# Kernel optimization log

Measured on AMD Instinct MI355X. Metric: run time of the kernel, lower is better.

## Reference

```python
import jax, jax.numpy as jnp
import numpy as np

DIM = 2048
N_HEADS = 16
N_KV_HEADS = 4
HEAD_DIM = DIM // N_HEADS  # 128
N_REP = N_HEADS // N_KV_HEADS  # 4
SEQ = 2048
BATCH = 2


def apply_rope(x, cos, sin):
    # x: [b, s, h, d]; cos/sin: [s, d//2]
    xr = x[..., 0::2]
    xi = x[..., 1::2]
    c = cos[None, :, None, :]
    s = sin[None, :, None, :]
    out_r = xr * c - xi * s
    out_i = xr * s + xi * c
    # interleave back: stack on last axis then flatten
    out = jnp.stack([out_r, out_i], axis=-1)
    return out.reshape(x.shape)


def setup_inputs() -> dict:
    key = jax.random.key(0)
    ks = jax.random.split(key, 7)
    x = jax.random.normal(ks[0], (BATCH, SEQ, DIM), dtype=jnp.float32)
    # realistic rotary tables
    inv_freq = 1.0 / (10000.0 ** (np.arange(0, HEAD_DIM, 2, dtype=np.float32) / HEAD_DIM))
    t = np.arange(SEQ, dtype=np.float32)
    freqs = np.outer(t, inv_freq)  # [S, d//2]
    freqs_cos = jnp.asarray(np.cos(freqs))
    freqs_sin = jnp.asarray(np.sin(freqs))
    sc = 0.02
    Wq = jax.random.normal(ks[1], (DIM, N_HEADS * HEAD_DIM), dtype=jnp.float32) * sc
    Wk = jax.random.normal(ks[2], (DIM, N_KV_HEADS * HEAD_DIM), dtype=jnp.float32) * sc
    Wv = jax.random.normal(ks[3], (DIM, N_KV_HEADS * HEAD_DIM), dtype=jnp.float32) * sc
    Wo = jax.random.normal(ks[4], (N_HEADS * HEAD_DIM, DIM), dtype=jnp.float32) * sc
    return {"x": x, "freqs_cos": freqs_cos, "freqs_sin": freqs_sin,
            "Wq": Wq, "Wk": Wk, "Wv": Wv, "Wo": Wo}


def reference(x, freqs_cos, freqs_sin, Wq, Wk, Wv, Wo):
    b, s, _ = x.shape
    xq = (x @ Wq).reshape(b, s, N_HEADS, HEAD_DIM)
    xk = (x @ Wk).reshape(b, s, N_KV_HEADS, HEAD_DIM)
    xv = (x @ Wv).reshape(b, s, N_KV_HEADS, HEAD_DIM)
    xq = apply_rope(xq, freqs_cos, freqs_sin)
    xk = apply_rope(xk, freqs_cos, freqs_sin)
    # GQA attention without materializing repeated KV:
    # group query heads as [b, g, r, s, d] with g=N_KV_HEADS, r=N_REP
    q = xq.reshape(b, s, N_KV_HEADS, N_REP, HEAD_DIM)
    scale = 1.0 / jnp.sqrt(jnp.float32(HEAD_DIM))
    scores = jnp.einsum('bqgrd,bkgd->bgrqk', q, xk) * scale  # [b,g,r,s,s]
    causal = jnp.tril(jnp.ones((s, s), dtype=bool))
    scores = jnp.where(causal[None, None, None], scores, jnp.finfo(scores.dtype).min)
    probs = jax.nn.softmax(scores, axis=-1)
    out = jnp.einsum('bgrqk,bkgd->bqgrd', probs, xv)  # [b,s,g,r,d]
    out = out.reshape(b, s, N_HEADS * HEAD_DIM)
    return out @ Wo
```

## Files before the change

### kernel.cpp

```cpp
#include <hip/hip_runtime.h>
#include <stdint.h>
#include <stddef.h>

constexpr int BATCH = 2;
constexpr int SEQ   = 2048;
constexpr int EMB   = 2048;
constexpr int HEADS = 16;
constexpr int GQA   = 4;
constexpr int HDIM  = 128;
constexpr int NQKV  = 3072;
constexpr int VOFF  = 2560;
constexpr int MROWS = BATCH * SEQ;

typedef _Float16 half8  __attribute__((ext_vector_type(8)));
typedef _Float16 half4v __attribute__((ext_vector_type(4)));
typedef float    floatx4 __attribute__((ext_vector_type(4)));

__device__ __forceinline__ void st_c(float* p, float v)    { *p = v; }
__device__ __forceinline__ void st_c(_Float16* p, float v) { *p = (_Float16)v; }

__device__ __forceinline__ void gld16(const _Float16* g, _Float16* l) {
    __builtin_amdgcn_global_load_lds(
        (const __attribute__((address_space(1))) void*)g,
        (__attribute__((address_space(3))) void*)l, 16, 0, 0);
}

__global__ void cast_x_kernel(const float* __restrict__ x, _Float16* __restrict__ xh) {
    int i = (blockIdx.x * 256 + threadIdx.x) * 4;
    float4 v = *(const float4*)(x + i);
    half4v h;
    h[0] = (_Float16)v.x; h[1] = (_Float16)v.y; h[2] = (_Float16)v.z; h[3] = (_Float16)v.w;
    *(half4v*)(xh + i) = h;
}

__global__ void transpose_cast(const float* __restrict__ in, _Float16* __restrict__ out,
                               int R, int C) {
    __shared__ float tile[32][33];
    int cb = blockIdx.x * 32, rb = blockIdx.y * 32;
    int tx = threadIdx.x, ty = threadIdx.y;
    #pragma unroll
    for (int j = 0; j < 32; j += 8)
        tile[ty + j][tx] = in[(size_t)(rb + ty + j) * C + (cb + tx)];
    __syncthreads();
    #pragma unroll
    for (int j = 0; j < 32; j += 8)
        out[(size_t)(cb + ty + j) * R + (rb + tx)] = (_Float16)tile[tx][ty + j];
}

template <typename CT, bool ROPE>
__global__ __launch_bounds__(256) void gemm_bt(const _Float16* __restrict__ A,
                                               const _Float16* __restrict__ Bt,
                                               CT* __restrict__ C,
                                               int M, int N, int K,
                                               const float* __restrict__ fc,
                                               const float* __restrict__ fs) {
    constexpr int LDT = 40;
    __shared__ _Float16 As[128 * LDT];
    __shared__ _Float16 Bs[128 * LDT];
    const int tid  = threadIdx.x;
    const int bm   = blockIdx.y * 128, bn = blockIdx.x * 128;
    const int lane = tid & 63, wid = tid >> 6;
    const int wr   = wid >> 1, wc = wid & 1;
    const int qd   = lane >> 4, m15 = lane & 15;

    const int sr = tid >> 2;
    const int sc = (tid & 3) * 8;
    const _Float16* Ag  = A  + (size_t)(bm + sr) * K + sc;
    const _Float16* Ag2 = Ag + (size_t)64 * K;
    const _Float16* Bg  = Bt + (size_t)(bn + sr) * K + sc;
    const _Float16* Bg2 = Bg + (size_t)64 * K;

    half8 a0 = *(const half8*)(Ag);
    half8 a1 = *(const half8*)(Ag2);
    half8 b0 = *(const half8*)(Bg);
    half8 b1 = *(const half8*)(Bg2);

    floatx4 acc[4][4] = {};

    _Float16* AsW  = As + sr * LDT + sc;
    _Float16* AsW2 = AsW + 64 * LDT;
    _Float16* BsW  = Bs + sr * LDT + sc;
    _Float16* BsW2 = BsW + 64 * LDT;
    const _Float16* AsR = As + (wr * 64 + m15) * LDT + qd * 8;
    const _Float16* BsR = Bs + (wc * 64 + m15) * LDT + qd * 8;

    for (int k0 = 0; k0 < K; k0 += 32) {
        *(half8*)AsW  = a0;  *(half8*)AsW2 = a1;
        *(half8*)BsW  = b0;  *(half8*)BsW2 = b1;
        __syncthreads();
        if (k0 + 32 < K) {
            a0 = *(const half8*)(Ag  + k0 + 32);
            a1 = *(const half8*)(Ag2 + k0 + 32);
            b0 = *(const half8*)(Bg  + k0 + 32);
            b1 = *(const half8*)(Bg2 + k0 + 32);
        }
        half8 af[4], bf[4];
        #pragma unroll
        for (int i = 0; i < 4; i++) af[i] = *(const half8*)(AsR + i * 16 * LDT);
        #pragma unroll
        for (int i = 0; i < 4; i++) bf[i] = *(const half8*)(BsR + i * 16 * LDT);
        #pragma unroll
        for (int mi = 0; mi < 4; mi++)
            #pragma unroll
            for (int ni = 0; ni < 4; ni++)
                acc[mi][ni] = __builtin_amdgcn_mfma_f32_16x16x32_f16(af[mi], bf[ni], acc[mi][ni], 0, 0, 0);
        __syncthreads();
    }

    #pragma unroll
    for (int mi = 0; mi < 4; mi++)
        #pragma unroll
        for (int ni = 0; ni < 4; ni++)
            #pragma unroll
            for (int r = 0; r < 4; r++) {
                int row = bm + wr * 64 + mi * 16 + qd * 4 + r;
                int col = bn + wc * 64 + ni * 16 + m15;
                float v = acc[mi][ni][r];
                if (ROPE && col < VOFF) {
                    int si = row & (SEQ - 1);
                    int fi = (col >> 1) & 63;
                    float c  = fc[si * 64 + fi];
                    float sn = fs[si * 64 + fi];
                    float other = __shfl_xor(v, 1, 64);
                    v = (m15 & 1) ? (v * c + other * sn) : (v * c - other * sn);
                }
                st_c(&C[(size_t)row * N + col], v);
            }
}

__global__ void transpose_v(const _Float16* __restrict__ qkv, _Float16* __restrict__ vt) {
    __shared__ _Float16 tile[32][33];
    int sb = blockIdx.x * 32, db = blockIdx.y * 32;
    int bg = blockIdx.z;
    int tx = threadIdx.x, ty = threadIdx.y;
    const _Float16* src = qkv + (size_t)(bg >> 2) * SEQ * NQKV + VOFF + (bg & 3) * HDIM;
    #pragma unroll
    for (int j = 0; j < 32; j += 8)
        tile[ty + j][tx] = src[(size_t)(sb + ty + j) * NQKV + db + tx];
    __syncthreads();
    _Float16* dst = vt + (size_t)bg * HDIM * SEQ;
    #pragma unroll
    for (int j = 0; j < 32; j += 8)
        dst[(size_t)(db + ty + j) * SEQ + sb + tx] = tile[tx][ty + j];
}

__global__ __launch_bounds__(256, 1) void flash_attn(const _Float16* __restrict__ qkv,
                                                     const _Float16* __restrict__ vt,
                                                     _Float16* __restrict__ ob) {
    const int bx   = blockIdx.x;
    const int g    = blockIdx.y;
    const int b    = blockIdx.z;
    const int tid  = threadIdx.x;
    const int lane = tid & 63, wid = tid >> 6;
    const int h    = g * 4 + wid;
    const int qd   = lane >> 4, m15 = lane & 15;

    __shared__ _Float16 Ks[2][64 * 128];
    __shared__ _Float16 Vs[2][128 * 64];
    __shared__ _Float16 Ps[4][32 * 64];

    const _Float16* kg = qkv + (size_t)(b * SEQ) * NQKV + EMB + g * HDIM;
    const _Float16* vg = vt + (size_t)(b * GQA + g) * HDIM * SEQ;
    _Float16* pw = Ps[wid];

    const int kl = lane >> 4, kc16 = lane & 15;
    const int vl = lane >> 3, vc8  = lane & 7;
    const _Float16* kgp[4]; const _Float16* vgp[4];
    int ksoff[4], vsoff[4];
    #pragma unroll
    for (int j = 0; j < 4; j++) {
        int t = wid * 4 + j;
        int kr = t * 4 + kl;
        kgp[j] = kg + (size_t)kr * NQKV + ((kc16 ^ (kr & 15)) * 8);
        ksoff[j] = t * 512;
        int vr = t * 8 + vl;
        vgp[j] = vg + (size_t)vr * SEQ + ((vc8 ^ (vr & 7)) * 8);
        vsoff[j] = t * 512;
    }

    half8 ones;
    #pragma unroll
    for (int i = 0; i < 8; i++) ones[i] = (_Float16)1.0f;
    const _Float16 qsc = (_Float16)(0.08838834764831845f * 1.44269504088896341f);

    for (int ph = 0; ph < 2; ++ph) {
        const int sidx   = ph ? bx : 63 - bx;
        const int q0     = sidx * 32;
        const int ktLast = sidx >> 1;

        __syncthreads();
        #pragma unroll
        for (int j = 0; j < 4; j++) gld16(kgp[j], &Ks[0][ksoff[j]]);
        #pragma unroll
        for (int j = 0; j < 4; j++) gld16(vgp[j], &Vs[0][vsoff[j]]);

        half8 qf[2][4];
        #pragma unroll
        for (int su = 0; su < 2; su++) {
            const _Float16* qb = qkv + (size_t)(b * SEQ + q0 + su * 16 + m15) * NQKV + h * HDIM + qd * 8;
            #pragma unroll
            for (int kc = 0; kc < 4; kc++) {
                half8 q = *(const half8*)(qb + kc * 32);
                #pragma unroll
                for (int i = 0; i < 8; i++) q[i] = (_Float16)(q[i] * qsc);
                qf[su][kc] = q;
            }
        }

        floatx4 o[2][9] = {};

        for (int kt = 0; kt <= ktLast; ++kt) {
            const int cur = kt & 1;
            __syncthreads();
            if (kt < ktLast) {
                const int nb = cur ^ 1;
                const size_t ko = (size_t)(kt + 1) * 64;
                #pragma unroll
                for (int j = 0; j < 4; j++) gld16(kgp[j] + ko * NQKV, &Ks[nb][ksoff[j]]);
                #pragma unroll
                for (int j = 0; j < 4; j++) gld16(vgp[j] + ko, &Vs[nb][vsoff[j]]);
            }
            const _Float16* ksb = Ks[cur];
            const _Float16* vsb = Vs[cur];

            floatx4 sa[2][4] = {};
            #pragma unroll
            for (int nt = 0; nt < 4; ++nt) {
                const int kr = nt * 16 + m15;
                #pragma unroll
                for (int kc = 0; kc < 4; ++kc) {
                    half8 kf = *(const half8*)(&ksb[kr * 128 + (((kc * 4 + qd) ^ (kr & 15)) * 8)]);
                    sa[0][nt] = __builtin_amdgcn_mfma_f32_16x16x32_f16(qf[0][kc], kf, sa[0][nt], 0, 0, 0);
                    sa[1][nt] = __builtin_amdgcn_mfma_f32_16x16x32_f16(qf[1][kc], kf, sa[1][nt], 0, 0, 0);
                }
            }

            const bool diag = (kt == ktLast);
            const int  k0   = kt * 64;
            #pragma unroll
            for (int su = 0; su < 2; su++)
                #pragma unroll
                for (int r = 0; r < 4; r++) {
                    const int prow = su * 16 + qd * 4 + r;
                    #pragma unroll
                    for (int nt = 0; nt < 4; nt++) {
                        float p = __builtin_exp2f(sa[su][nt][r]);
                        if (diag && (k0 + nt * 16 + m15 > q0 + prow)) p = 0.f;
                        int chunk = (nt * 2 + (m15 >> 3)) ^ (prow & 7);
                        pw[prow * 64 + chunk * 8 + (m15 & 7)] = (_Float16)p;
                    }
                }

            half8 pf[2][2];
            #pragma unroll
            for (int su = 0; su < 2; su++)
                #pragma unroll
                for (int kc = 0; kc < 2; kc++) {
                    int prow = su * 16 + m15;
                    pf[su][kc] = *(const half8*)(&pw[prow * 64 + (((kc * 4 + qd) ^ (prow & 7)) * 8)]);
                }
            #pragma unroll
            for (int dt = 0; dt < 8; dt++) {
                const int vr = dt * 16 + m15;
                #pragma unroll
                for (int kc = 0; kc < 2; kc++) {
                    half8 vf = *(const half8*)(&vsb[vr * 64 + (((kc * 4 + qd) ^ (vr & 7)) * 8)]);
                    o[0][dt] = __builtin_amdgcn_mfma_f32_16x16x32_f16(pf[0][kc], vf, o[0][dt], 0, 0, 0);
                    o[1][dt] = __builtin_amdgcn_mfma_f32_16x16x32_f16(pf[1][kc], vf, o[1][dt], 0, 0, 0);
                }
            }
            #pragma unroll
            for (int su = 0; su < 2; su++) {
                o[su][8] = __builtin_amdgcn_mfma_f32_16x16x32_f16(pf[su][0], ones, o[su][8], 0, 0, 0);
                o[su][8] = __builtin_amdgcn_mfma_f32_16x16x32_f16(pf[su][1], ones, o[su][8], 0, 0, 0);
            }
        }

        #pragma unroll
        for (int su = 0; su < 2; su++) {
            float linv[4];
            #pragma unroll
            for (int r = 0; r < 4; r++) linv[r] = 1.0f / o[su][8][r];
            _Float16* od = ob + (size_t)(b * SEQ + q0 + su * 16) * EMB + h * HDIM;
            #pragma unroll
            for (int dt = 0; dt < 8; dt++)
                #pragma unroll
                for (int r = 0; r < 4; r++)
                    od[(size_t)(qd * 4 + r) * EMB + dt * 16 + m15] = (_Float16)(o[su][dt][r] * linv[r]);
        }
    }
}

extern "C" void kernel_launch(void* const* d_in, const int* in_sizes, int n_in,
                              void* d_out, int out_size, void* d_ws, size_t ws_size,
                              hipStream_t stream) {
    (void)in_sizes; (void)n_in; (void)out_size; (void)ws_size;
    const float* x  = (const float*)d_in[0];
    const float* fc = (const float*)d_in[1];
    const float* fs = (const float*)d_in[2];
    const float* Wq = (const float*)d_in[3];
    const float* Wk = (const float*)d_in[4];
    const float* Wv = (const float*)d_in[5];
    const float* Wo = (const float*)d_in[6];
    float* out = (float*)d_out;

    _Float16* Xb   = (_Float16*)d_ws;
    _Float16* Wqkv = Xb   + (size_t)MROWS * EMB;
    _Float16* WoT  = Wqkv + (size_t)NQKV * EMB;
    _Float16* C1   = WoT  + (size_t)EMB * EMB;
    _Float16* Vt   = Wqkv;
    _Float16* Ob   = Xb;

    dim3 tb(32, 8);
    cast_x_kernel<<<MROWS * EMB / 1024, 256, 0, stream>>>(x, Xb);
    transpose_cast<<<dim3(EMB / 32, EMB / 32), tb, 0, stream>>>(Wq, Wqkv, EMB, EMB);
    transpose_cast<<<dim3(512 / 32, EMB / 32), tb, 0, stream>>>(Wk, Wqkv + (size_t)EMB * EMB, EMB, 512);
    transpose_cast<<<dim3(512 / 32, EMB / 32), tb, 0, stream>>>(Wv, Wqkv + (size_t)VOFF * EMB, EMB, 512);
    transpose_cast<<<dim3(EMB / 32, EMB / 32), tb, 0, stream>>>(Wo, WoT, EMB, EMB);

    gemm_bt<_Float16, true><<<dim3(NQKV / 128, MROWS / 128), 256, 0, stream>>>(
        Xb, Wqkv, C1, MROWS, NQKV, EMB, fc, fs);
    transpose_v<<<dim3(SEQ / 32, HDIM / 32, BATCH * GQA), tb, 0, stream>>>(C1, Vt);
    flash_attn<<<dim3(32, GQA, BATCH), 256, 0, stream>>>(C1, Vt, Ob);
    gemm_bt<float, false><<<dim3(EMB / 128, MROWS / 128), 256, 0, stream>>>(
        Ob, WoT, out, MROWS, EMB, EMB, nullptr, nullptr);
}
```

Before: 351.9 us.

## Split flash attention query rows across 8 waves per block

```diff
diff --git a/kernel.cpp b/kernel.cpp
--- a/kernel.cpp
+++ b/kernel.cpp
@@ -144,7 +144,7 @@
         dst[(size_t)(db + ty + j) * SEQ + sb + tx] = tile[tx][ty + j];
 }
 
-__global__ __launch_bounds__(256, 1) void flash_attn(const _Float16* __restrict__ qkv,
+__global__ __launch_bounds__(512, 2) void flash_attn(const _Float16* __restrict__ qkv,
                                                      const _Float16* __restrict__ vt,
                                                      _Float16* __restrict__ ob) {
     const int bx   = blockIdx.x;
@@ -152,12 +152,13 @@
     const int b    = blockIdx.z;
     const int tid  = threadIdx.x;
     const int lane = tid & 63, wid = tid >> 6;
-    const int h    = g * 4 + wid;
+    const int h    = g * 4 + (wid & 3);
+    const int su   = wid >> 2;
     const int qd   = lane >> 4, m15 = lane & 15;
 
     __shared__ _Float16 Ks[2][64 * 128];
     __shared__ _Float16 Vs[2][128 * 64];
-    __shared__ _Float16 Ps[4][32 * 64];
+    __shared__ _Float16 Ps[8][16 * 64];
 
     const _Float16* kg = qkv + (size_t)(b * SEQ) * NQKV + EMB + g * HDIM;
     const _Float16* vg = vt + (size_t)(b * GQA + g) * HDIM * SEQ;
@@ -165,11 +166,11 @@
 
     const int kl = lane >> 4, kc16 = lane & 15;
     const int vl = lane >> 3, vc8  = lane & 7;
-    const _Float16* kgp[4]; const _Float16* vgp[4];
-    int ksoff[4], vsoff[4];
-    #pragma unroll
-    for (int j = 0; j < 4; j++) {
-        int t = wid * 4 + j;
+    const _Float16* kgp[2]; const _Float16* vgp[2];
+    int ksoff[2], vsoff[2];
+    #pragma unroll
+    for (int j = 0; j < 2; j++) {
+        int t = wid * 2 + j;
         int kr = t * 4 + kl;
         kgp[j] = kg + (size_t)kr * NQKV + ((kc16 ^ (kr & 15)) * 8);
         ksoff[j] = t * 512;
@@ -190,24 +191,23 @@
 
         __syncthreads();
         #pragma unroll
-        for (int j = 0; j < 4; j++) gld16(kgp[j], &Ks[0][ksoff[j]]);
-        #pragma unroll
-        for (int j = 0; j < 4; j++) gld16(vgp[j], &Vs[0][vsoff[j]]);
-
-        half8 qf[2][4];
-        #pragma unroll
-        for (int su = 0; su < 2; su++) {
+        for (int j = 0; j < 2; j++) gld16(kgp[j], &Ks[0][ksoff[j]]);
+        #pragma unroll
+        for (int j = 0; j < 2; j++) gld16(vgp[j], &Vs[0][vsoff[j]]);
+
+        half8 qf[4];
+        {
             const _Float16* qb = qkv + (size_t)(b * SEQ + q0 + su * 16 + m15) * NQKV + h * HDIM + qd * 8;
             #pragma unroll
             for (int kc = 0; kc < 4; kc++) {
                 half8 q = *(const half8*)(qb + kc * 32);
                 #pragma unroll
                 for (int i = 0; i < 8; i++) q[i] = (_Float16)(q[i] * qsc);
-                qf[su][kc] = q;
+                qf[kc] = q;
             }
         }
 
-        floatx4 o[2][9] = {};
+        floatx4 o[9] = {};
 
         for (int kt = 0; kt <= ktLast; ++kt) {
             const int cur = kt & 1;
@@ -216,78 +216,66 @@
                 const int nb = cur ^ 1;
                 const size_t ko = (size_t)(kt + 1) * 64;
                 #pragma unroll
-                for (int j = 0; j < 4; j++) gld16(kgp[j] + ko * NQKV, &Ks[nb][ksoff[j]]);
-                #pragma unroll
-                for (int j = 0; j < 4; j++) gld16(vgp[j] + ko, &Vs[nb][vsoff[j]]);
+                for (int j = 0; j < 2; j++) gld16(kgp[j] + ko * NQKV, &Ks[nb][ksoff[j]]);
+                #pragma unroll
+                for (int j = 0; j < 2; j++) gld16(vgp[j] + ko, &Vs[nb][vsoff[j]]);
             }
             const _Float16* ksb = Ks[cur];
             const _Float16* vsb = Vs[cur];
 
-            floatx4 sa[2][4] = {};
+            floatx4 sa[4] = {};
             #pragma unroll
             for (int nt = 0; nt < 4; ++nt) {
                 const int kr = nt * 16 + m15;
                 #pragma unroll
                 for (int kc = 0; kc < 4; ++kc) {
                     half8 kf = *(const half8*)(&ksb[kr * 128 + (((kc * 4 + qd) ^ (kr & 15)) * 8)]);
-                    sa[0][nt] = __builtin_amdgcn_mfma_f32_16x16x32_f16(qf[0][kc], kf, sa[0][nt], 0, 0, 0);
-                    sa[1][nt] = __builtin_amdgcn_mfma_f32_16x16x32_f16(qf[1][kc], kf, sa[1][nt], 0, 0, 0);
+                    sa[nt] = __builtin_amdgcn_mfma_f32_16x16x32_f16(qf[kc], kf, sa[nt], 0, 0, 0);
                 }
             }
 
             const bool diag = (kt == ktLast);
             const int  k0   = kt * 64;
             #pragma unroll
-            for (int su = 0; su < 2; su++)
-                #pragma unroll
-                for (int r = 0; r < 4; r++) {
-                    const int prow = su * 16 + qd * 4 + r;
-                    #pragma unroll
-                    for (int nt = 0; nt < 4; nt++) {
-                        float p = __builtin_exp2f(sa[su][nt][r]);
-                        if (diag && (k0 + nt * 16 + m15 > q0 + prow)) p = 0.f;
-                        int chunk = (nt * 2 + (m15 >> 3)) ^ (prow & 7);
-                        pw[prow * 64 + chunk * 8 + (m15 & 7)] = (_Float16)p;
-                    }
+            for (int r = 0; r < 4; r++) {
+                const int prow = qd * 4 + r;
+                const int rowg = q0 + su * 16 + prow;
+                #pragma unroll
+                for (int nt = 0; nt < 4; nt++) {
+                    float p = __builtin_exp2f(sa[nt][r]);
+                    if (diag && (k0 + nt * 16 + m15 > rowg)) p = 0.f;
+                    int chunk = (nt * 2 + (m15 >> 3)) ^ (prow & 7);
+                    pw[prow * 64 + chunk * 8 + (m15 & 7)] = (_Float16)p;
                 }
-
-            half8 pf[2][2];
-            #pragma unroll
-            for (int su = 0; su < 2; su++)
-                #pragma unroll
-                for (int kc = 0; kc < 2; kc++) {
-                    int prow = su * 16 + m15;
-                    pf[su][kc] = *(const half8*)(&pw[prow * 64 + (((kc * 4 + qd) ^ (prow & 7)) * 8)]);
-                }
+            }
+
+            half8 pf[2];
+            #pragma unroll
+            for (int kc = 0; kc < 2; kc++)
+                pf[kc] = *(const half8*)(&pw[m15 * 64 + (((kc * 4 + qd) ^ (m15 & 7)) * 8)]);
+
             #pragma unroll
             for (int dt = 0; dt < 8; dt++) {
                 const int vr = dt * 16 + m15;
                 #pragma unroll
                 for (int kc = 0; kc < 2; kc++) {
                     half8 vf = *(const half8*)(&vsb[vr * 64 + (((kc * 4 + qd) ^ (vr & 7)) * 8)]);
-                    o[0][dt] = __builtin_amdgcn_mfma_f32_16x16x32_f16(pf[0][kc], vf, o[0][dt], 0, 0, 0);
-                    o[1][dt] = __builtin_amdgcn_mfma_f32_16x16x32_f16(pf[1][kc], vf, o[1][dt], 0, 0, 0);
+                    o[dt] = __builtin_amdgcn_mfma_f32_16x16x32_f16(pf[kc], vf, o[dt], 0, 0, 0);
                 }
             }
-            #pragma unroll
-            for (int su = 0; su < 2; su++) {
-                o[su][8] = __builtin_amdgcn_mfma_f32_16x16x32_f16(pf[su][0], ones, o[su][8], 0, 0, 0);
-                o[su][8] = __builtin_amdgcn_mfma_f32_16x16x32_f16(pf[su][1], ones, o[su][8], 0, 0, 0);
-            }
+            o[8] = __builtin_amdgcn_mfma_f32_16x16x32_f16(pf[0], ones, o[8], 0, 0, 0);
+            o[8] = __builtin_amdgcn_mfma_f32_16x16x32_f16(pf[1], ones, o[8], 0, 0, 0);
         }
 
-        #pragma unroll
-        for (int su = 0; su < 2; su++) {
-            float linv[4];
-            #pragma unroll
-            for (int r = 0; r < 4; r++) linv[r] = 1.0f / o[su][8][r];
-            _Float16* od = ob + (size_t)(b * SEQ + q0 + su * 16) * EMB + h * HDIM;
-            #pragma unroll
-            for (int dt = 0; dt < 8; dt++)
-                #pragma unroll
-                for (int r = 0; r < 4; r++)
-                    od[(size_t)(qd * 4 + r) * EMB + dt * 16 + m15] = (_Float16)(o[su][dt][r] * linv[r]);
-        }
+        float linv[4];
+        #pragma unroll
+        for (int r = 0; r < 4; r++) linv[r] = 1.0f / o[8][r];
+        _Float16* od = ob + (size_t)(b * SEQ + q0 + su * 16) * EMB + h * HDIM;
+        #pragma unroll
+        for (int dt = 0; dt < 8; dt++)
+            #pragma unroll
+            for (int r = 0; r < 4; r++)
+                od[(size_t)(qd * 4 + r) * EMB + dt * 16 + m15] = (_Float16)(o[dt][r] * linv[r]);
     }
 }
 
@@ -321,7 +309,7 @@
     gemm_bt<_Float16, true><<<dim3(NQKV / 128, MROWS / 128), 256, 0, stream>>>(
         Xb, Wqkv, C1, MROWS, NQKV, EMB, fc, fs);
     transpose_v<<<dim3(SEQ / 32, HDIM / 32, BATCH * GQA), tb, 0, stream>>>(C1, Vt);
-    flash_attn<<<dim3(32, GQA, BATCH), 256, 0, stream>>>(C1, Vt, Ob);
+    flash_attn<<<dim3(32, GQA, BATCH), 512, 0, stream>>>(C1, Vt, Ob);
     gemm_bt<float, false><<<dim3(EMB / 128, MROWS / 128), 256, 0, stream>>>(
         Ob, WoT, out, MROWS, EMB, EMB, nullptr, nullptr);
 }
```

Result: faster. 319.9 us (-9.1%).
